# Performance work log

Hardware: AMD Instinct MI355X
Metric: run time of the kernel (lower is better)

## Reference

```python
import jax, jax.numpy as jnp
import numpy as np


def setup_inputs() -> dict:
    key = jax.random.key(0)
    ks = jax.random.split(key, 5)
    B, S, I, H = 64, 512, 1024, 1024
    s_ih = 1.0 / np.sqrt(I)
    s_hh = 1.0 / np.sqrt(H)
    return {
        "x": jax.random.normal(ks[0], (B, S, I), dtype=jnp.float32),
        "W_ih": jax.random.normal(ks[1], (H, I), dtype=jnp.float32) * s_ih,
        "b_ih": jax.random.normal(ks[2], (H,), dtype=jnp.float32) * s_ih,
        "W_hh": jax.random.normal(ks[3], (H, H), dtype=jnp.float32) * s_hh,
        "b_hh": jax.random.normal(ks[4], (H,), dtype=jnp.float32) * s_hh,
    }


def reference(x, W_ih, b_ih, W_hh, b_hh):
    # x: (B, S, I). Precompute the input projection for all timesteps in one GEMM.
    B, S, _ = x.shape
    H = W_hh.shape[0]
    xi = jnp.einsum("bsi,hi->bsh", x, W_ih) + b_ih  # (B, S, H)

    def step(h, xt):  # xt: (B, H)
        h_new = jnp.tanh(xt + h @ W_hh.T + b_hh)
        return h_new, h_new

    h0 = jnp.zeros((B, H), dtype=x.dtype)
    h_final, outs = jax.lax.scan(step, h0, jnp.swapaxes(xi, 0, 1))  # outs: (S, B, H)
    # Faithful to torch source: torch.cat(output, dim=0) stacks time-major
    # (S*B, H), then .view(bs, seq, H) reinterprets that buffer row-major.
    output = outs.reshape(B, S, H)
    return output, h_final
```

## Files before the change

### kernel.cpp

```cpp
#include <hip/hip_runtime.h>
#include <math.h>

#define BB 64
#define SS 512
#define II 1024
#define HH 1024

typedef _Float16 half8  __attribute__((ext_vector_type(8)));
typedef _Float16 half4_t __attribute__((ext_vector_type(4)));
typedef float    float4_t __attribute__((ext_vector_type(4)));

#define XH_OFF   0u
#define WIH_OFF  67108864u
#define WHH_OFF  69206016u
#define HBUF_OFF 71303168u
#define FLG_OFF  71565312u

__device__ __forceinline__ void load_lds16(const void* g, void* l) {
  __builtin_amdgcn_global_load_lds(
      (const __attribute__((address_space(1))) void*)g,
      (__attribute__((address_space(3))) void*)l, 16, 0, 0);
}

__global__ __launch_bounds__(256) void convert_kernel(
    const float* __restrict__ x, const float* __restrict__ Wih,
    const float* __restrict__ Whh, _Float16* __restrict__ xh,
    _Float16* __restrict__ Wihh, _Float16* __restrict__ Whhh,
    unsigned* __restrict__ flg) {
  long tid = (long)blockIdx.x * blockDim.x + threadIdx.x;
  if (tid < 1024) flg[tid] = 0;
  if (tid < 8388608L) {
    long f = tid;
    int i4 = (int)(f & 255);
    int s  = (int)((f >> 8) & 511);
    int b  = (int)(f >> 17);
    float4_t v = ((const float4_t*)x)[f];
    half4_t h;
    h[0] = (_Float16)v[0]; h[1] = (_Float16)v[1];
    h[2] = (_Float16)v[2]; h[3] = (_Float16)v[3];
    long dst = ((long)(s * 64 + b) * 1024 + i4 * 4) >> 2;
    ((half4_t*)xh)[dst] = h;
  } else if (tid < 8388608L + 262144L) {
    long f = tid - 8388608L;
    float4_t v = ((const float4_t*)Wih)[f];
    half4_t h;
    h[0] = (_Float16)v[0]; h[1] = (_Float16)v[1];
    h[2] = (_Float16)v[2]; h[3] = (_Float16)v[3];
    ((half4_t*)Wihh)[f] = h;
  } else if (tid < 8388608L + 524288L) {
    long f = tid - 8388608L - 262144L;
    float4_t v = ((const float4_t*)Whh)[f];
    half4_t h;
    h[0] = (_Float16)v[0]; h[1] = (_Float16)v[1];
    h[2] = (_Float16)v[2]; h[3] = (_Float16)v[3];
    ((half4_t*)Whhh)[f] = h;
  }
}

__global__ __launch_bounds__(256) void gemm_xi(
    const _Float16* __restrict__ Ap, const _Float16* __restrict__ Bp,
    const float* __restrict__ bias, float* __restrict__ out) {
  __shared__ _Float16 Al[128 * 32];
  __shared__ _Float16 Bl[128 * 32];
  int bid = blockIdx.x;
  int nT = bid & 7, mT = bid >> 3;
  int tid = threadIdx.x;
  int lane = tid & 63, wv = tid >> 6;
  int wm = wv & 1, wn = wv >> 1;
  int nl = lane & 15, quad = lane >> 4;
  long mBase = (long)mT * 128;
  long nBase = (long)nT * 128;
  float4_t acc[4][4] = {};

  for (int k0 = 0; k0 < 1024; k0 += 32) {
    __syncthreads();
#pragma unroll
    for (int c2 = 0; c2 < 2; ++c2) {
      int c = wv * 2 + c2;
      int flat = c * 64 + lane;
      int row = flat >> 2;
      int off = (flat & 3) * 8;
      load_lds16(Ap + (mBase + row) * 1024 + k0 + off, &Al[c * 512]);
      load_lds16(Bp + (nBase + row) * 1024 + k0 + off, &Bl[c * 512]);
    }
    __syncthreads();
    half8 af[4], bf[4];
#pragma unroll
    for (int t = 0; t < 4; ++t) {
      af[t] = *(const half8*)&Al[(wm * 64 + t * 16 + nl) * 32 + quad * 8];
      bf[t] = *(const half8*)&Bl[(wn * 64 + t * 16 + nl) * 32 + quad * 8];
    }
#pragma unroll
    for (int tm = 0; tm < 4; ++tm)
#pragma unroll
      for (int tn = 0; tn < 4; ++tn)
        acc[tm][tn] = __builtin_amdgcn_mfma_f32_16x16x32_f16(
            af[tm], bf[tn], acc[tm][tn], 0, 0, 0);
  }
#pragma unroll
  for (int tm = 0; tm < 4; ++tm) {
    long rowg = mBase + wm * 64 + tm * 16 + quad * 4;
#pragma unroll
    for (int tn = 0; tn < 4; ++tn) {
      long colg = nBase + wn * 64 + tn * 16 + nl;
      float bi = bias[colg];
#pragma unroll
      for (int r = 0; r < 4; ++r)
        out[(rowg + r) * 1024 + colg] = acc[tm][tn][r] + bi;
    }
  }
}

__global__ __launch_bounds__(256, 1) void rnn_rec(
    const _Float16* __restrict__ Whh, const float* __restrict__ bhh,
    float* __restrict__ out, _Float16* __restrict__ hbuf,
    unsigned* __restrict__ flags) {
  __shared__ __align__(16) float red[2][4][4][2][256];
  __shared__ __align__(16) _Float16 hstage[4][512];
  const int slice = blockIdx.x;
  const int tid = threadIdx.x;
  const int wv = tid >> 6, lane = tid & 63;
  const int nl = lane & 15, quad = lane >> 4;
  const int colbase = slice * 32;

  half8 wfrag[2][8];
#pragma unroll
  for (int n = 0; n < 2; ++n)
#pragma unroll
    for (int t = 0; t < 8; ++t)
      wfrag[n][t] = *(const half8*)(Whh + (long)(colbase + n * 16 + nl) * 1024 +
                                    wv * 256 + t * 32 + quad * 8);

  const int mycol0 = colbase + nl, mycol1 = colbase + 16 + nl;
  const float bi0 = bhh[mycol0], bi1 = bhh[mycol1];
  const int mybat = wv * 16 + quad * 4;
  const int ri = nl * 16 + quad * 4;

#pragma unroll 1
  for (int s = 0; s < 512; ++s) {
    float xi0[4], xi1[4];
#pragma unroll
    for (int r = 0; r < 4; ++r) {
      long rowo = ((long)s * 64 + mybat + r) * 1024;
      xi0[r] = out[rowo + mycol0];
      xi1[r] = out[rowo + mycol1];
    }

    float4_t acc[4][2] = {};
    if (s > 0) {
      {
        const unsigned widx = ((unsigned)(wv * 32 + (lane & 31))) << 3;
        while (true) {
          unsigned f = __hip_atomic_load(&flags[widx], __ATOMIC_RELAXED,
                                         __HIP_MEMORY_SCOPE_AGENT);
          if (__ballot(f < (unsigned)s) == 0ull) break;
          __builtin_amdgcn_s_sleep(1);
        }
      }
      const _Float16* hb = hbuf + ((s - 1) & 1) * 65536 + wv * 256 + quad * 8;
      float4_t hf[4][8];
      __builtin_amdgcn_sched_barrier(0);
#pragma unroll
      for (int m = 0; m < 4; ++m)
#pragma unroll
        for (int t = 0; t < 8; ++t)
          asm volatile("global_load_dwordx4 %0, %1, off sc0 sc1"
                       : "=v"(hf[m][t])
                       : "v"(hb + ((m * 16 + nl) << 10) + t * 32));
      asm volatile("s_waitcnt vmcnt(0)" ::: "memory");
      __builtin_amdgcn_sched_barrier(0);
#pragma unroll
      for (int t = 0; t < 8; ++t)
#pragma unroll
        for (int m = 0; m < 4; ++m) {
          half8 a = __builtin_bit_cast(half8, hf[m][t]);
          acc[m][0] = __builtin_amdgcn_mfma_f32_16x16x32_f16(
              a, wfrag[0][t], acc[m][0], 0, 0, 0);
          acc[m][1] = __builtin_amdgcn_mfma_f32_16x16x32_f16(
              a, wfrag[1][t], acc[m][1], 0, 0, 0);
        }
    }

#pragma unroll
    for (int m = 0; m < 4; ++m)
#pragma unroll
      for (int n = 0; n < 2; ++n)
        *(float4_t*)&red[s & 1][wv][m][n][ri] = acc[m][n];
    __syncthreads();
    float4_t fin0, fin1;
    {
      float4_t a0 = *(const float4_t*)&red[s & 1][0][wv][0][ri];
      float4_t b0 = *(const float4_t*)&red[s & 1][1][wv][0][ri];
      float4_t c0 = *(const float4_t*)&red[s & 1][2][wv][0][ri];
      float4_t d0 = *(const float4_t*)&red[s & 1][3][wv][0][ri];
      fin0 = (a0 + b0) + (c0 + d0);
      float4_t a1 = *(const float4_t*)&red[s & 1][0][wv][1][ri];
      float4_t b1 = *(const float4_t*)&red[s & 1][1][wv][1][ri];
      float4_t c1 = *(const float4_t*)&red[s & 1][2][wv][1][ri];
      float4_t d1 = *(const float4_t*)&red[s & 1][3][wv][1][ri];
      fin1 = (a1 + b1) + (c1 + d1);
    }

    float hv0[4], hv1[4];
#pragma unroll
    for (int r = 0; r < 4; ++r) {
      float pre0 = fin0[r] + xi0[r] + bi0;
      float e0 = __expf(2.f * pre0);
      float v0 = 1.f - 2.f / (e0 + 1.f);
      hv0[r] = v0;
      hstage[wv][(quad * 4 + r) * 32 + nl] = (_Float16)v0;
      float pre1 = fin1[r] + xi1[r] + bi1;
      float e1 = __expf(2.f * pre1);
      float v1 = 1.f - 2.f / (e1 + 1.f);
      hv1[r] = v1;
      hstage[wv][(quad * 4 + r) * 32 + 16 + nl] = (_Float16)v1;
    }
    {
      float4_t pv = *(const float4_t*)&hstage[wv][(lane >> 2) * 32 + (lane & 3) * 8];
      _Float16* dst = hbuf + (s & 1) * 65536 +
                      ((wv * 16 + (lane >> 2)) << 10) + colbase + (lane & 3) * 8;
      asm volatile("global_store_dwordx4 %0, %1, off sc0 sc1"
                   :: "v"(dst), "v"(pv) : "memory");
      asm volatile("s_waitcnt vmcnt(0)" ::: "memory");
      if (lane == 0)
        __hip_atomic_store(&flags[((unsigned)(slice * 4 + wv)) << 3],
                           (unsigned)(s + 1), __ATOMIC_RELAXED,
                           __HIP_MEMORY_SCOPE_AGENT);
    }

#pragma unroll
    for (int r = 0; r < 4; ++r) {
      long rowo = ((long)s * 64 + mybat + r) * 1024;
      out[rowo + mycol0] = hv0[r];
      out[rowo + mycol1] = hv1[r];
      if (s == 511) {
        out[33554432L + (mybat + r) * 1024 + mycol0] = hv0[r];
        out[33554432L + (mybat + r) * 1024 + mycol1] = hv1[r];
      }
    }
  }
}

extern "C" void kernel_launch(void* const* d_in, const int* in_sizes, int n_in,
                              void* d_out, int out_size, void* d_ws,
                              size_t ws_size, hipStream_t stream) {
  const float* x   = (const float*)d_in[0];
  const float* Wih = (const float*)d_in[1];
  const float* bih = (const float*)d_in[2];
  const float* Whh = (const float*)d_in[3];
  const float* bhh = (const float*)d_in[4];
  char* ws = (char*)d_ws;
  _Float16* xh   = (_Float16*)(ws + XH_OFF);
  _Float16* Wihh = (_Float16*)(ws + WIH_OFF);
  _Float16* Whhh = (_Float16*)(ws + WHH_OFF);
  _Float16* hbuf = (_Float16*)(ws + HBUF_OFF);
  unsigned* flg  = (unsigned*)(ws + FLG_OFF);
  float* out = (float*)d_out;

  convert_kernel<<<34816, 256, 0, stream>>>(x, Wih, Whh, xh, Wihh, Whhh, flg);
  gemm_xi<<<2048, 256, 0, stream>>>(xh, Wihh, bih, out);
  rnn_rec<<<32, 256, 0, stream>>>(Whhh, bhh, out, hbuf, flg);
}
```

Measured before the change: 3.423 ms.

## Replace per-step flag polling with sentinel-poisoned quad-buffered hidden state

The recurrent kernel no longer publishes a per-wave flag after each step. Consumers instead poll the hidden-state buffer itself until no all-ones (NaN) sentinel words remain. The buffer is expanded to four slots, and each step re-poisons the slot two ahead. This removes the store-wait plus separate flag round trip from the critical path, at the cost of repeated full-tile reloads while spinning, an initial grid-wide barrier, and reuse of the xh workspace region for the buffers. The reduction layout index ri also changes.

Result: slower. 3.704 ms (+8.2%).

```diff
diff --git a/kernel.cpp b/kernel.cpp
--- a/kernel.cpp
+++ b/kernel.cpp
@@ -9,11 +9,11 @@
 typedef _Float16 half8  __attribute__((ext_vector_type(8)));
 typedef _Float16 half4_t __attribute__((ext_vector_type(4)));
 typedef float    float4_t __attribute__((ext_vector_type(4)));
+typedef unsigned uint4v  __attribute__((ext_vector_type(4)));
 
 #define XH_OFF   0u
 #define WIH_OFF  67108864u
 #define WHH_OFF  69206016u
-#define HBUF_OFF 71303168u
 #define FLG_OFF  71565312u
 
 __device__ __forceinline__ void load_lds16(const void* g, void* l) {
@@ -131,10 +131,35 @@
       wfrag[n][t] = *(const half8*)(Whh + (long)(colbase + n * 16 + nl) * 1024 +
                                     wv * 256 + t * 32 + quad * 8);
 
+  const float4_t pz = __builtin_bit_cast(float4_t, (uint4v){~0u, ~0u, ~0u, ~0u});
+  {
+    int row = tid >> 2, ch = tid & 3;
+#pragma unroll
+    for (int b = 0; b < 4; ++b) {
+      _Float16* pd = hbuf + b * 65536 + (row << 10) + colbase + ch * 8;
+      asm volatile("global_store_dwordx4 %0, %1, off sc0 sc1"
+                   :: "v"(pd), "v"(pz) : "memory");
+    }
+  }
+  asm volatile("s_waitcnt vmcnt(0)" ::: "memory");
+  __syncthreads();
+  if (tid == 0)
+    __hip_atomic_store(&flags[(unsigned)slice << 5], 1u, __ATOMIC_RELAXED,
+                       __HIP_MEMORY_SCOPE_AGENT);
+  if (wv == 0) {
+    while (true) {
+      unsigned f = __hip_atomic_load(&flags[(unsigned)(lane & 31) << 5],
+                                     __ATOMIC_RELAXED, __HIP_MEMORY_SCOPE_AGENT);
+      if (__ballot(f == 0u) == 0ull) break;
+      __builtin_amdgcn_s_sleep(1);
+    }
+  }
+  __syncthreads();
+
   const int mycol0 = colbase + nl, mycol1 = colbase + 16 + nl;
   const float bi0 = bhh[mycol0], bi1 = bhh[mycol1];
   const int mybat = wv * 16 + quad * 4;
-  const int ri = nl * 16 + quad * 4;
+  const int ri = quad * 64 + nl * 4;
 
 #pragma unroll 1
   for (int s = 0; s < 512; ++s) {
@@ -148,26 +173,33 @@
 
     float4_t acc[4][2] = {};
     if (s > 0) {
-      {
-        const unsigned widx = ((unsigned)(wv * 32 + (lane & 31))) << 3;
-        while (true) {
-          unsigned f = __hip_atomic_load(&flags[widx], __ATOMIC_RELAXED,
-                                         __HIP_MEMORY_SCOPE_AGENT);
-          if (__ballot(f < (unsigned)s) == 0ull) break;
-          __builtin_amdgcn_s_sleep(1);
-        }
+      const _Float16* hb = hbuf + ((s - 1) & 3) * 65536 + wv * 256 + quad * 8;
+      float4_t hf[4][8];
+      while (true) {
+        __builtin_amdgcn_sched_barrier(0);
+#pragma unroll
+        for (int m = 0; m < 4; ++m)
+#pragma unroll
+          for (int t = 0; t < 8; ++t)
+            asm volatile("global_load_dwordx4 %0, %1, off sc0 sc1"
+                         : "=v"(hf[m][t])
+                         : "v"(hb + ((m * 16 + nl) << 10) + t * 32));
+        asm volatile("s_waitcnt vmcnt(0)" ::: "memory");
+        __builtin_amdgcn_sched_barrier(0);
+        unsigned mx = 0u;
+#pragma unroll
+        for (int m = 0; m < 4; ++m)
+#pragma unroll
+          for (int t = 0; t < 8; ++t) {
+            uint4v u = __builtin_bit_cast(uint4v, hf[m][t]);
+            unsigned a = u[0] > u[1] ? u[0] : u[1];
+            unsigned b = u[2] > u[3] ? u[2] : u[3];
+            unsigned c = a > b ? a : b;
+            mx = c > mx ? c : mx;
+          }
+        if (__ballot(mx == 0xFFFFFFFFu) == 0ull) break;
+        __builtin_amdgcn_s_sleep(0);
       }
-      const _Float16* hb = hbuf + ((s - 1) & 1) * 65536 + wv * 256 + quad * 8;
-      float4_t hf[4][8];
-      __builtin_amdgcn_sched_barrier(0);
-#pragma unroll
-      for (int m = 0; m < 4; ++m)
-#pragma unroll
-        for (int t = 0; t < 8; ++t)
-          asm volatile("global_load_dwordx4 %0, %1, off sc0 sc1"
-                       : "=v"(hf[m][t])
-                       : "v"(hb + ((m * 16 + nl) << 10) + t * 32));
-      asm volatile("s_waitcnt vmcnt(0)" ::: "memory");
       __builtin_amdgcn_sched_barrier(0);
 #pragma unroll
       for (int t = 0; t < 8; ++t)
@@ -217,15 +249,16 @@
     }
     {
       float4_t pv = *(const float4_t*)&hstage[wv][(lane >> 2) * 32 + (lane & 3) * 8];
-      _Float16* dst = hbuf + (s & 1) * 65536 +
+      _Float16* dst = hbuf + (s & 3) * 65536 +
                       ((wv * 16 + (lane >> 2)) << 10) + colbase + (lane & 3) * 8;
       asm volatile("global_store_dwordx4 %0, %1, off sc0 sc1"
                    :: "v"(dst), "v"(pv) : "memory");
-      asm volatile("s_waitcnt vmcnt(0)" ::: "memory");
-      if (lane == 0)
-        __hip_atomic_store(&flags[((unsigned)(slice * 4 + wv)) << 3],
-                           (unsigned)(s + 1), __ATOMIC_RELAXED,
-                           __HIP_MEMORY_SCOPE_AGENT);
+    }
+    {
+      int row = tid >> 2, ch = tid & 3;
+      _Float16* pd = hbuf + ((s + 2) & 3) * 65536 + (row << 10) + colbase + ch * 8;
+      asm volatile("global_store_dwordx4 %0, %1, off sc0 sc1"
+                   :: "v"(pd), "v"(pz) : "memory");
     }
 
 #pragma unroll
@@ -253,7 +286,7 @@
   _Float16* xh   = (_Float16*)(ws + XH_OFF);
   _Float16* Wihh = (_Float16*)(ws + WIH_OFF);
   _Float16* Whhh = (_Float16*)(ws + WHH_OFF);
-  _Float16* hbuf = (_Float16*)(ws + HBUF_OFF);
+  _Float16* hbuf = (_Float16*)(ws + XH_OFF);
   unsigned* flg  = (unsigned*)(ws + FLG_OFF);
   float* out = (float*)d_out;
 
```
